# Optimization experiments

Hardware: AMD Instinct MI355X
Metric: run time of the kernel (lower is better)

## Reference

```python
import jax, jax.numpy as jnp
import numpy as np

B, S, E, H, FF = 4, 2048, 1024, 16, 4096
TD = 32  # transition_dim


def _layer_norm(v, g, b, eps=1e-5):
    m = v.mean(-1, keepdims=True)
    var = ((v - m) ** 2).mean(-1, keepdims=True)
    return (v - m) * jax.lax.rsqrt(var + eps) * g + b


def setup_inputs() -> dict:
    key = jax.random.key(0)
    ks = jax.random.split(key, 8)
    w = 0.02
    return {
        "x": jax.random.normal(ks[0], (B, S, E), dtype=jnp.float32),
        "transition_dim": TD,
        "ln1_g": jnp.ones((E,), jnp.float32),
        "ln1_b": jnp.zeros((E,), jnp.float32),
        "ln2_g": jnp.ones((E,), jnp.float32),
        "ln2_b": jnp.zeros((E,), jnp.float32),
        "w_qkv": jax.random.normal(ks[1], (3 * E, E), jnp.float32) * w,
        "b_qkv": jnp.zeros((3 * E,), jnp.float32),
        "w_o": jax.random.normal(ks[2], (E, E), jnp.float32) * w,
        "b_o": jnp.zeros((E,), jnp.float32),
        "w_fc1": jax.random.normal(ks[3], (FF, E), jnp.float32) * w,
        "b_fc1": jnp.zeros((FF,), jnp.float32),
        "w_fc2": jax.random.normal(ks[4], (E, FF), jnp.float32) * w,
        "b_fc2": jnp.zeros((E,), jnp.float32),
    }


def reference(x, transition_dim, ln1_g, ln1_b, ln2_g, ln2_b, w_qkv, b_qkv,
              w_o, b_o, w_fc1, b_fc1, w_fc2, b_fc2):
    Bx, Sx, Ex = x.shape
    Dh = Ex // H
    xn = _layer_norm(x, ln1_g, ln1_b)
    qkv = xn @ w_qkv.T + b_qkv                      # [B,S,3E]
    q, k, v = jnp.split(qkv, 3, axis=-1)
    def heads(t):
        return t.reshape(Bx, Sx, H, Dh).transpose(0, 2, 1, 3)  # [B,H,S,Dh]
    q, k, v = heads(q), heads(k), heads(v)
    scores = jnp.einsum("bhqd,bhkd->bhqk", q, k) / np.sqrt(Dh).astype(np.float32)
    # custom mask: causal (j > i) OR periodic value-column (j % TD == TD-1) blocked
    i = jnp.arange(Sx)
    mask = (i[None, :] > i[:, None]) | ((i[None, :] % transition_dim) == transition_dim - 1)
    scores = jnp.where(mask[None, None], -jnp.inf, scores)
    p = jax.nn.softmax(scores, axis=-1)
    attn = jnp.einsum("bhqk,bhkd->bhqd", p, v)
    attn = attn.transpose(0, 2, 1, 3).reshape(Bx, Sx, Ex)
    attn = attn @ w_o.T + b_o
    x = x + attn
    h = _layer_norm(x, ln2_g, ln2_b)
    h = jax.nn.gelu(h @ w_fc1.T + b_fc1, approximate=False) @ w_fc2.T + b_fc2
    return x + h
```

## Files before the change

kernel.cpp:

```cpp
#include <hip/hip_runtime.h>
#include <hip/hip_bf16.h>

typedef unsigned short u16;
typedef unsigned int u32;
typedef short bf16x8 __attribute__((ext_vector_type(8)));
typedef float f32x4 __attribute__((ext_vector_type(4)));
typedef float f32x16 __attribute__((ext_vector_type(16)));

#define B_ 4
#define S_ 2048
#define E_ 1024
#define H_ 16
#define FF_ 4096
#define M_ 8192

__device__ __forceinline__ u16 f2bf(float f) {
    u32 u = __float_as_uint(f);
    u32 r = (u + 0x7FFFu + ((u >> 16) & 1u)) >> 16;
    return (u16)r;
}
__device__ __forceinline__ float bf2f(u16 v) {
    return __uint_as_float(((u32)v) << 16);
}
__device__ __forceinline__ u32 cvtpk(float lo, float hi) {
    u32 r;
    asm("v_cvt_pk_bf16_f32 %0, %1, %2" : "=v"(r) : "v"(lo), "v"(hi));
    return r;
}
__device__ __forceinline__ void pswap(u32& a, u32& b) {
    asm("v_permlane32_swap_b32 %0, %1" : "+v"(a), "+v"(b));
}

__device__ __forceinline__ void gload16(const void* g, void* l) {
    __builtin_amdgcn_global_load_lds(
        (__attribute__((address_space(1))) void*)g,
        (__attribute__((address_space(3))) void*)l, 16, 0, 0);
}

__global__ __launch_bounds__(256) void cvt_kernel(const float* __restrict__ in,
                                                  u16* __restrict__ out, int n4) {
    int i = blockIdx.x * 256 + threadIdx.x;
    if (i < n4) {
        float4 v = ((const float4*)in)[i];
        ushort4 o;
        o.x = f2bf(v.x); o.y = f2bf(v.y); o.z = f2bf(v.z); o.w = f2bf(v.w);
        ((ushort4*)out)[i] = o;
    }
}

__global__ __launch_bounds__(256) void ln_kernel(const float* __restrict__ x,
                                                 const float* __restrict__ g,
                                                 const float* __restrict__ bb,
                                                 u16* __restrict__ out) {
    int row = blockIdx.x;
    int t = threadIdx.x;
    const float4* xr = (const float4*)(x + (size_t)row * E_);
    float4 v = xr[t];
    float s = v.x + v.y + v.z + v.w;
    float sq = v.x * v.x + v.y * v.y + v.z * v.z + v.w * v.w;
    for (int o = 1; o < 64; o <<= 1) {
        s += __shfl_xor(s, o, 64);
        sq += __shfl_xor(sq, o, 64);
    }
    __shared__ float ss[4], sqs[4];
    int w = t >> 6, l = t & 63;
    if (l == 0) { ss[w] = s; sqs[w] = sq; }
    __syncthreads();
    s = ss[0] + ss[1] + ss[2] + ss[3];
    sq = sqs[0] + sqs[1] + sqs[2] + sqs[3];
    float mean = s * (1.0f / E_);
    float var = sq * (1.0f / E_) - mean * mean;
    float rstd = rsqrtf(var + 1e-5f);
    float4 gv = ((const float4*)g)[t];
    float4 bv = ((const float4*)bb)[t];
    ushort4 o4;
    o4.x = f2bf((v.x - mean) * rstd * gv.x + bv.x);
    o4.y = f2bf((v.y - mean) * rstd * gv.y + bv.y);
    o4.z = f2bf((v.z - mean) * rstd * gv.z + bv.z);
    o4.w = f2bf((v.w - mean) * rstd * gv.w + bv.w);
    ((ushort4*)(out + (size_t)row * E_))[t] = o4;
}

template <int EPI, int BN>
__global__ __launch_bounds__(512, 2) void gemm256(const u16* __restrict__ A,
                                                  const u16* __restrict__ Bt,
                                                  const float* __restrict__ bias,
                                                  void* __restrict__ outp,
                                                  const float* __restrict__ resid,
                                                  int N, int K) {
    constexpr int NF = BN / 64;
    __shared__ u16 ldsA[2 * 2 * 8192];
    __shared__ u16 ldsB[BN == 256 ? 2 * 2 * 8192 : 2 * 8192];
    int t = threadIdx.x;
    int wid = t >> 6, l = t & 63, l15 = l & 15, hi4 = l >> 4;
    int wm = wid >> 2, wn = wid & 3;

    int nwg = gridDim.x;
    int flat = blockIdx.x;
    int swz = (flat & 7) * (nwg >> 3) + (flat >> 3);
    int nx = N / BN;
    int m0 = (swz / nx) * 256, n0 = (swz % nx) * BN;
    const size_t Kb = (size_t)K * 2;

    f32x4 acc[8][NF];
    f32x4 zf = {0.f, 0.f, 0.f, 0.f};
#pragma unroll
    for (int i = 0; i < 8; i++)
#pragma unroll
        for (int j = 0; j < NF; j++) acc[i][j] = zf;

    auto stageA = [&](int buf, int h, int k0) {
#pragma unroll
        for (int rr = 0; rr < 2; ++rr) {
            int o = t * 16 + rr * 8192;
            int lr = o >> 7;
            int gch = ((o >> 4) & 7) ^ (lr & 7);
            int grow = m0 + (lr >> 6) * 128 + h * 64 + (lr & 63);
            gload16((const char*)A + (size_t)grow * Kb + k0 * 2 + gch * 16,
                    (char*)ldsA + (buf * 2 + h) * 16384 + o);
        }
    };
    auto stageB256 = [&](int buf, int h, int k0) {
#pragma unroll
        for (int rr = 0; rr < 2; ++rr) {
            int o = t * 16 + rr * 8192;
            int lr = o >> 7;
            int gch = ((o >> 4) & 7) ^ (lr & 7);
            int grow = n0 + (lr >> 5) * 64 + h * 32 + (lr & 31);
            gload16((const char*)Bt + (size_t)grow * Kb + k0 * 2 + gch * 16,
                    (char*)ldsB + (buf * 2 + h) * 16384 + o);
        }
    };
    auto stageB128 = [&](int buf, int k0) {
#pragma unroll
        for (int rr = 0; rr < 2; ++rr) {
            int o = t * 16 + rr * 8192;
            int lr = o >> 7;
            int gch = ((o >> 4) & 7) ^ (lr & 7);
            int grow = n0 + lr;
            gload16((const char*)Bt + (size_t)grow * Kb + k0 * 2 + gch * 16,
                    (char*)ldsB + buf * 16384 + o);
        }
    };

    auto readA = [&](int bq, int mh, bf16x8 (&af)[4][2]) {
#pragma unroll
        for (int mi = 0; mi < 4; mi++)
#pragma unroll
            for (int ks = 0; ks < 2; ks++) {
                int lr = wm * 64 + mi * 16 + l15;
                int ob = lr * 128 + ks * 64 + hi4 * 16;
                af[mi][ks] = *(const bf16x8*)((const char*)ldsA +
                             (bq * 2 + mh) * 16384 + (ob ^ ((lr & 7) << 4)));
            }
    };
    auto readB256 = [&](int bq, int nh, bf16x8 (&bfr)[2][2]) {
#pragma unroll
        for (int nq = 0; nq < 2; nq++)
#pragma unroll
            for (int ks = 0; ks < 2; ks++) {
                int lr = wn * 32 + nq * 16 + l15;
                int ob = lr * 128 + ks * 64 + hi4 * 16;
                bfr[nq][ks] = *(const bf16x8*)((const char*)ldsB +
                              (bq * 2 + nh) * 16384 + (ob ^ ((lr & 7) << 4)));
            }
    };
    auto readB128 = [&](int bq, bf16x8 (&bfr)[2][2]) {
#pragma unroll
        for (int nq = 0; nq < 2; nq++)
#pragma unroll
            for (int ks = 0; ks < 2; ks++) {
                int lr = wn * 32 + nq * 16 + l15;
                int ob = lr * 128 + ks * 64 + hi4 * 16;
                bfr[nq][ks] = *(const bf16x8*)((const char*)ldsB +
                              bq * 16384 + (ob ^ ((lr & 7) << 4)));
            }
    };
    auto mma = [&](bf16x8 (&af)[4][2], bf16x8 (&bfr)[2][2], int mh, int nh) {
#pragma unroll
        for (int mi = 0; mi < 4; mi++)
#pragma unroll
            for (int nq = 0; nq < 2; nq++)
#pragma unroll
                for (int ks = 0; ks < 2; ks++)
                    acc[mh * 4 + mi][nh * 2 + nq] =
                        __builtin_amdgcn_mfma_f32_16x16x32_bf16(
                            af[mi][ks], bfr[nq][ks], acc[mh * 4 + mi][nh * 2 + nq], 0, 0, 0);
    };

#define GWAIT(N)                                            \
    asm volatile("s_waitcnt vmcnt(" #N ")" ::: "memory");   \
    __builtin_amdgcn_sched_barrier(0);
#define PH_MID                                              \
    __builtin_amdgcn_s_barrier();                           \
    asm volatile("s_waitcnt lgkmcnt(0)" ::: "memory");      \
    __builtin_amdgcn_sched_barrier(0);                      \
    __builtin_amdgcn_s_setprio(1);
#define PH_END                                              \
    __builtin_amdgcn_s_setprio(0);                          \
    __builtin_amdgcn_s_barrier();

    int KT = K >> 6, ITERS = KT >> 1;

    if constexpr (BN == 256) {
        stageB256(0, 0, 0); stageB256(0, 1, 0); stageA(0, 0, 0); stageA(0, 1, 0);
        stageB256(1, 0, 64); stageB256(1, 1, 64); stageA(1, 0, 64);
        GWAIT(6);
        __builtin_amdgcn_s_barrier();
        for (int s = 0; s < ITERS; ++s) {
            int k1 = (2 * s + 1) << 6;
            int k2 = (2 * s + 2) << 6; if (k2 >= K) k2 = 0;
            int k3 = (2 * s + 3) << 6; if (k3 >= K) k3 = 0;
            bf16x8 af[4][2], b0[2][2], b1[2][2];
            readA(0, 0, af); readB256(0, 0, b0); stageA(1, 1, k1);
            PH_MID; mma(af, b0, 0, 0); PH_END;
            readB256(0, 1, b1); stageB256(0, 0, k2);
            PH_MID; mma(af, b1, 0, 1); PH_END;
            readA(0, 1, af); stageB256(0, 1, k2);
            PH_MID; mma(af, b0, 1, 0); PH_END;
            stageA(0, 0, k2); GWAIT(6);
            PH_MID; mma(af, b1, 1, 1); PH_END;
            readA(1, 0, af); readB256(1, 0, b0); stageA(0, 1, k2);
            PH_MID; mma(af, b0, 0, 0); PH_END;
            readB256(1, 1, b1); stageB256(1, 0, k3);
            PH_MID; mma(af, b1, 0, 1); PH_END;
            readA(1, 1, af); stageB256(1, 1, k3);
            PH_MID; mma(af, b0, 1, 0); PH_END;
            stageA(1, 0, k3); GWAIT(6);
            PH_MID; mma(af, b1, 1, 1); PH_END;
        }
    } else {
        stageB128(0, 0); stageA(0, 0, 0); stageA(0, 1, 0);
        stageB128(1, 64); stageA(1, 0, 64);
        GWAIT(4);
        __builtin_amdgcn_s_barrier();
        for (int s = 0; s < ITERS; ++s) {
            int k1 = (2 * s + 1) << 6;
            int k2 = (2 * s + 2) << 6; if (k2 >= K) k2 = 0;
            int k3 = (2 * s + 3) << 6; if (k3 >= K) k3 = 0;
            bf16x8 af[4][2], br[2][2];
            readA(0, 0, af); readB128(0, br); stageA(1, 1, k1);
            PH_MID; mma(af, br, 0, 0); PH_END;
            readA(0, 1, af); stageB128(0, k2); stageA(0, 0, k2); GWAIT(4);
            PH_MID; mma(af, br, 1, 0); PH_END;
            readA(1, 0, af); readB128(1, br); stageA(0, 1, k2);
            PH_MID; mma(af, br, 0, 0); PH_END;
            readA(1, 1, af); stageB128(1, k3); stageA(1, 0, k3); GWAIT(4);
            PH_MID; mma(af, br, 1, 0); PH_END;
        }
    }
#undef GWAIT
#undef PH_MID
#undef PH_END

    float bias_v[NF];
#pragma unroll
    for (int nf = 0; nf < NF; nf++) bias_v[nf] = bias[n0 + wn * (NF * 16) + nf * 16 + l15];

#pragma unroll
    for (int mf = 0; mf < 8; mf++)
#pragma unroll
        for (int nf = 0; nf < NF; nf++)
#pragma unroll
            for (int j = 0; j < 4; j++) {
                int row = m0 + wm * 128 + mf * 16 + hi4 * 4 + j;
                int col = n0 + wn * (NF * 16) + nf * 16 + l15;
                float v = acc[mf][nf][j] + bias_v[nf];
                size_t idx = (size_t)row * N + col;
                if (EPI == 2) v = 0.5f * v * (1.0f + erff(v * 0.70710678118f));
                if (EPI == 1)
                    ((float*)outp)[idx] = resid[idx] + v;
                else
                    ((u16*)outp)[idx] = f2bf(v);
            }
}

__global__ __launch_bounds__(128) void attn_kernel(const u16* __restrict__ qkv,
                                                   u16* __restrict__ aout) {
    __shared__ u16 Ks[64 * 64];
    __shared__ u16 Vt[64 * 64];
    int t = threadIdx.x;
    int wv = t >> 6, l = t & 63;
    int q31 = l & 31, hi = l >> 5;
    int flat = blockIdx.x;
    int logical = (flat & 7) * 256 + (flat >> 3);
    int bh = logical >> 5;
    int qt = 31 - (logical & 31);
    int b = bh >> 4, h = bh & 15;
    int rowq = qt * 64 + wv * 32 + q31;

    const float qs = 0.18033688011f;
    const float THR = 44.3616f;

    bf16x8 qreg[4];
    const u16* qbase = qkv + (size_t)(b * S_ + rowq) * 3072 + h * 64 + hi * 8;
#pragma unroll
    for (int g = 0; g < 4; g++) qreg[g] = *(const bf16x8*)(qbase + 16 * g);

    f32x16 zf16;
#pragma unroll
    for (int r = 0; r < 16; r++) zf16[r] = 0.f;
    f32x16 o0 = zf16, o1 = zf16;
    float mrun = -INFINITY, lrun = 0.f;

    for (int jt = 0; jt <= qt; ++jt) {
        int j0 = jt * 64;
        __syncthreads();
#pragma unroll
        for (int pp = 0; pp < 4; pp++) {
            int oo = 16 * t + 2048 * pp;
            int row = oo >> 7, colb = oo & 127;
            const u16* src = qkv + E_ + (size_t)(b * S_ + j0 + row) * 3072 + h * 64 + (colb >> 1);
            uint4 d16 = *(const uint4*)src;
            int el = (((row << 6) + (colb >> 1)) ^ ((row & 7) << 3));
            *(uint4*)&Ks[el] = d16;
        }
#pragma unroll
        for (int pp = 0; pp < 4; pp++) {
            int db = wv + 2 * pp;
            const u16* src = qkv + 2 * E_ + (size_t)(b * S_ + j0 + l) * 3072 + h * 64 + db * 8;
            uint4 d16 = *(const uint4*)src;
            u32 uu[4] = {d16.x, d16.y, d16.z, d16.w};
#pragma unroll
            for (int e = 0; e < 8; e++) {
                u16 raw = (e & 1) ? (u16)(uu[e >> 1] >> 16) : (u16)(uu[e >> 1] & 0xffffu);
                int d = db * 8 + e;
                Vt[((d << 6) + l) ^ ((d & 7) << 3)] = raw;
            }
        }
        __syncthreads();

        f32x16 s0 = zf16, s1 = zf16;
        __builtin_amdgcn_s_setprio(1);
#pragma unroll
        for (int g = 0; g < 4; g++) {
            int r0 = q31, r1 = 32 + q31;
            bf16x8 k0 = *(const bf16x8*)&Ks[((r0 << 6) + hi * 8 + 16 * g) ^ ((r0 & 7) << 3)];
            bf16x8 k1 = *(const bf16x8*)&Ks[((r1 << 6) + hi * 8 + 16 * g) ^ ((r1 & 7) << 3)];
            s0 = __builtin_amdgcn_mfma_f32_32x32x16_bf16(k0, qreg[g], s0, 0, 0, 0);
            s1 = __builtin_amdgcn_mfma_f32_32x32x16_bf16(k1, qreg[g], s1, 0, 0, 0);
        }
        __builtin_amdgcn_s_setprio(0);

        float mx = -INFINITY;
        int cb0 = j0 + 4 * hi;
        if (jt == qt) {
#pragma unroll
            for (int r = 0; r < 16; r++) {
                const int cc = (r & 3) + 8 * (r >> 2);
                float v0 = s0[r], v1 = s1[r];
                bool bad0 = (cb0 + cc > rowq) || (r == 15 && hi);
                bool bad1 = (cb0 + 32 + cc > rowq) || (r == 15 && hi);
                v0 = bad0 ? -INFINITY : v0;
                v1 = bad1 ? -INFINITY : v1;
                s0[r] = v0; s1[r] = v1;
                mx = fmaxf(mx, fmaxf(v0, v1));
            }
        } else {
#pragma unroll
            for (int r = 0; r < 16; r++) {
                float v0 = s0[r], v1 = s1[r];
                if (r == 15) {
                    v0 = hi ? -INFINITY : v0;
                    v1 = hi ? -INFINITY : v1;
                    s0[r] = v0; s1[r] = v1;
                }
                mx = fmaxf(mx, fmaxf(v0, v1));
            }
        }
        mx = fmaxf(mx, __shfl_xor(mx, 32, 64));

        bool dokeep = __all(mx <= mrun + THR);
        if (!dokeep) {
            float mnew = fmaxf(mrun, mx);
            float sc = __builtin_amdgcn_exp2f((mrun - mnew) * qs);
#pragma unroll
            for (int r = 0; r < 16; r++) { o0[r] *= sc; o1[r] *= sc; }
            lrun *= sc;
            mrun = mnew;
        }
        float mq = mrun * qs;

        float sa = 0.f, sb = 0.f, sc2 = 0.f, sd = 0.f;
#pragma unroll
        for (int r = 0; r < 16; r++) {
            float p0 = __builtin_amdgcn_exp2f(fmaf(s0[r], qs, -mq));
            float p1 = __builtin_amdgcn_exp2f(fmaf(s1[r], qs, -mq));
            s0[r] = p0; s1[r] = p1;
            if (r & 1) { sb += p0; sd += p1; } else { sa += p0; sc2 += p1; }
        }
        lrun += (sa + sb) + (sc2 + sd);

        bf16x8 pa[4];
#pragma unroll
        for (int g = 0; g < 4; g++) {
            const int bs = (g & 1) * 8;
            u32 wa, wb, wc, wd;
            if (g < 2) {
                wa = cvtpk(s0[bs + 0], s0[bs + 1]);
                wb = cvtpk(s0[bs + 4], s0[bs + 5]);
                wc = cvtpk(s0[bs + 2], s0[bs + 3]);
                wd = cvtpk(s0[bs + 6], s0[bs + 7]);
            } else {
                wa = cvtpk(s1[bs + 0], s1[bs + 1]);
                wb = cvtpk(s1[bs + 4], s1[bs + 5]);
                wc = cvtpk(s1[bs + 2], s1[bs + 3]);
                wd = cvtpk(s1[bs + 6], s1[bs + 7]);
            }
            pswap(wa, wb);
            pswap(wc, wd);
            union { u32 w[4]; bf16x8 f; } u;
            u.w[0] = wa; u.w[1] = wc; u.w[2] = wb; u.w[3] = wd;
            pa[g] = u.f;
        }

        __builtin_amdgcn_s_setprio(1);
#pragma unroll
        for (int g = 0; g < 4; g++) {
            int d0 = q31, d1 = 32 + q31;
            bf16x8 v0 = *(const bf16x8*)&Vt[((d0 << 6) + hi * 8 + 16 * g) ^ ((d0 & 7) << 3)];
            bf16x8 v1 = *(const bf16x8*)&Vt[((d1 << 6) + hi * 8 + 16 * g) ^ ((d1 & 7) << 3)];
            o0 = __builtin_amdgcn_mfma_f32_32x32x16_bf16(v0, pa[g], o0, 0, 0, 0);
            o1 = __builtin_amdgcn_mfma_f32_32x32x16_bf16(v1, pa[g], o1, 0, 0, 0);
        }
        __builtin_amdgcn_s_setprio(0);
    }

    lrun += __shfl_xor(lrun, 32, 64);
    float inv = 1.0f / lrun;
    u16* orow = aout + (size_t)(b * S_ + rowq) * E_ + h * 64 + 4 * hi;
#pragma unroll
    for (int r = 0; r < 16; r++) {
        const int cc = (r & 3) + 8 * (r >> 2);
        orow[cc] = f2bf(o0[r] * inv);
        orow[32 + cc] = f2bf(o1[r] * inv);
    }
}

extern "C" void kernel_launch(void* const* d_in, const int* in_sizes, int n_in,
                              void* d_out, int out_size, void* d_ws, size_t ws_size,
                              hipStream_t stream) {
    const float* x = (const float*)d_in[0];
    const float* ln1_g = (const float*)d_in[2];
    const float* ln1_b = (const float*)d_in[3];
    const float* ln2_g = (const float*)d_in[4];
    const float* ln2_b = (const float*)d_in[5];
    const float* w_qkv = (const float*)d_in[6];
    const float* b_qkv = (const float*)d_in[7];
    const float* w_o = (const float*)d_in[8];
    const float* b_o = (const float*)d_in[9];
    const float* w_fc1 = (const float*)d_in[10];
    const float* b_fc1 = (const float*)d_in[11];
    const float* w_fc2 = (const float*)d_in[12];
    const float* b_fc2 = (const float*)d_in[13];
    float* out = (float*)d_out;
    char* ws = (char*)d_ws;

    u16* wqkv_bf = (u16*)(ws);
    u16* wo_bf   = (u16*)(ws + 6291456);
    u16* wfc1_bf = (u16*)(ws + 8388608);
    u16* wfc2_bf = (u16*)(ws + 16777216);
    u16* xn_bf   = (u16*)(ws + 25165824);
    u16* qkv_bf  = (u16*)(ws + 41943040);
    u16* ffn1_bf = (u16*)(ws + 41943040);
    u16* attn_bf = (u16*)(ws + 92274688);
    float* x2    = (float*)(ws + 109051904);
    (void)in_sizes; (void)n_in; (void)out_size; (void)ws_size;

    cvt_kernel<<<3072, 256, 0, stream>>>(w_qkv, wqkv_bf, 786432);
    cvt_kernel<<<1024, 256, 0, stream>>>(w_o, wo_bf, 262144);
    cvt_kernel<<<4096, 256, 0, stream>>>(w_fc1, wfc1_bf, 1048576);
    cvt_kernel<<<4096, 256, 0, stream>>>(w_fc2, wfc2_bf, 1048576);

    ln_kernel<<<M_, 256, 0, stream>>>(x, ln1_g, ln1_b, xn_bf);

    gemm256<0, 256><<<384, 512, 0, stream>>>(xn_bf, wqkv_bf, b_qkv, qkv_bf, nullptr, 3072, 1024);

    attn_kernel<<<2048, 128, 0, stream>>>(qkv_bf, attn_bf);

    gemm256<1, 128><<<256, 512, 0, stream>>>(attn_bf, wo_bf, b_o, x2, x, 1024, 1024);

    ln_kernel<<<M_, 256, 0, stream>>>(x2, ln2_g, ln2_b, xn_bf);

    gemm256<2, 256><<<512, 512, 0, stream>>>(xn_bf, wfc1_bf, b_fc1, ffn1_bf, nullptr, 4096, 1024);

    gemm256<1, 128><<<256, 512, 0, stream>>>(ffn1_bf, wfc2_bf, b_fc2, out, x2, 1024, 4096);
}
```

Measured before the change: 404.6 us.

## Emit transposed V from QKV GEMM and double-buffer async K/V loads in attention

The QKV GEMM gets a new epilogue that also writes V in a transposed [B,H,Dh,S] layout into workspace (aliased with x2, which is only written after attention). The attention kernel drops its per-element V transpose into LDS and synchronous K loads. It now uses global_load_lds into double-buffered K/V tiles, prefetching two tiles ahead with vmcnt waits and barriers. This aims to overlap memory latency with MFMA work and remove scalar LDS scatter stores. The cost is extra global writes in the GEMM epilogue and twice the LDS per block.

```diff
diff --git a/kernel.cpp b/kernel.cpp
--- a/kernel.cpp
+++ b/kernel.cpp
@@ -30,7 +30,6 @@
 __device__ __forceinline__ void pswap(u32& a, u32& b) {
     asm("v_permlane32_swap_b32 %0, %1" : "+v"(a), "+v"(b));
 }
-
 __device__ __forceinline__ void gload16(const void* g, void* l) {
     __builtin_amdgcn_global_load_lds(
         (__attribute__((address_space(1))) void*)g,
@@ -87,6 +86,7 @@
                                                   const float* __restrict__ bias,
                                                   void* __restrict__ outp,
                                                   const float* __restrict__ resid,
+                                                  u16* __restrict__ vt,
                                                   int N, int K) {
     constexpr int NF = BN / 64;
     __shared__ u16 ldsA[2 * 2 * 8192];
@@ -257,28 +257,52 @@
 #pragma unroll
     for (int nf = 0; nf < NF; nf++) bias_v[nf] = bias[n0 + wn * (NF * 16) + nf * 16 + l15];
 
-#pragma unroll
-    for (int mf = 0; mf < 8; mf++)
-#pragma unroll
-        for (int nf = 0; nf < NF; nf++)
-#pragma unroll
-            for (int j = 0; j < 4; j++) {
-                int row = m0 + wm * 128 + mf * 16 + hi4 * 4 + j;
+    if constexpr (EPI == 3) {
+#pragma unroll
+        for (int mf = 0; mf < 8; mf++)
+#pragma unroll
+            for (int nf = 0; nf < NF; nf++) {
                 int col = n0 + wn * (NF * 16) + nf * 16 + l15;
-                float v = acc[mf][nf][j] + bias_v[nf];
-                size_t idx = (size_t)row * N + col;
-                if (EPI == 2) v = 0.5f * v * (1.0f + erff(v * 0.70710678118f));
-                if (EPI == 1)
-                    ((float*)outp)[idx] = resid[idx] + v;
-                else
-                    ((u16*)outp)[idx] = f2bf(v);
-            }
+                int row0 = m0 + wm * 128 + mf * 16 + hi4 * 4;
+                ushort4 sv;
+                u16* o16 = (u16*)outp;
+#pragma unroll
+                for (int j = 0; j < 4; j++) {
+                    float v = acc[mf][nf][j] + bias_v[nf];
+                    u16 r = f2bf(v);
+                    o16[(size_t)(row0 + j) * N + col] = r;
+                    ((u16*)&sv)[j] = r;
+                }
+                if (col >= 2048) {
+                    int bb = row0 >> 11, s0r = row0 & 2047;
+                    *(ushort4*)&vt[(((size_t)(bb << 10) + (col - 2048)) << 11) + s0r] = sv;
+                }
+            }
+    } else {
+#pragma unroll
+        for (int mf = 0; mf < 8; mf++)
+#pragma unroll
+            for (int nf = 0; nf < NF; nf++)
+#pragma unroll
+                for (int j = 0; j < 4; j++) {
+                    int row = m0 + wm * 128 + mf * 16 + hi4 * 4 + j;
+                    int col = n0 + wn * (NF * 16) + nf * 16 + l15;
+                    float v = acc[mf][nf][j] + bias_v[nf];
+                    size_t idx = (size_t)row * N + col;
+                    if (EPI == 2) v = 0.5f * v * (1.0f + erff(v * 0.70710678118f));
+                    if (EPI == 1)
+                        ((float*)outp)[idx] = resid[idx] + v;
+                    else
+                        ((u16*)outp)[idx] = f2bf(v);
+                }
+    }
 }
 
 __global__ __launch_bounds__(128) void attn_kernel(const u16* __restrict__ qkv,
+                                                   const u16* __restrict__ vt,
                                                    u16* __restrict__ aout) {
-    __shared__ u16 Ks[64 * 64];
-    __shared__ u16 Vt[64 * 64];
+    __shared__ u16 Ksb[2 * 4096];
+    __shared__ u16 Vsb[2 * 4096];
     int t = threadIdx.x;
     int wv = t >> 6, l = t & 63;
     int q31 = l & 31, hi = l >> 5;
@@ -297,46 +321,50 @@
 #pragma unroll
     for (int g = 0; g < 4; g++) qreg[g] = *(const bf16x8*)(qbase + 16 * g);
 
+    const char* srcK0 = (const char*)(qkv + E_ + (size_t)(b * S_ + (t >> 3)) * 3072 + h * 64) +
+                        ((t & 7) ^ ((t >> 3) & 7)) * 16;
+    const char* srcV0 = (const char*)(vt + ((size_t)(bh * 64 + (t >> 3))) * 2048) +
+                        ((t & 7) ^ ((t >> 3) & 7)) * 16;
+    auto issueK = [&](int buf, int j0) {
+#pragma unroll
+        for (int pp = 0; pp < 4; pp++)
+            gload16(srcK0 + (size_t)pp * 98304 + (size_t)j0 * 6144,
+                    (char*)Ksb + buf * 8192 + 16 * t + 2048 * pp);
+    };
+    auto issueV = [&](int buf, int j0) {
+#pragma unroll
+        for (int pp = 0; pp < 4; pp++)
+            gload16(srcV0 + (size_t)pp * 65536 + (size_t)j0 * 2,
+                    (char*)Vsb + buf * 8192 + 16 * t + 2048 * pp);
+    };
+
     f32x16 zf16;
 #pragma unroll
     for (int r = 0; r < 16; r++) zf16[r] = 0.f;
     f32x16 o0 = zf16, o1 = zf16;
     float mrun = -INFINITY, lrun = 0.f;
 
+    int j1 = (qt >= 1) ? 64 : 0;
+    issueK(0, 0); issueV(0, 0);
+    issueK(1, j1); issueV(1, j1);
+
     for (int jt = 0; jt <= qt; ++jt) {
+        int cur = jt & 1;
         int j0 = jt * 64;
-        __syncthreads();
-#pragma unroll
-        for (int pp = 0; pp < 4; pp++) {
-            int oo = 16 * t + 2048 * pp;
-            int row = oo >> 7, colb = oo & 127;
-            const u16* src = qkv + E_ + (size_t)(b * S_ + j0 + row) * 3072 + h * 64 + (colb >> 1);
-            uint4 d16 = *(const uint4*)src;
-            int el = (((row << 6) + (colb >> 1)) ^ ((row & 7) << 3));
-            *(uint4*)&Ks[el] = d16;
-        }
-#pragma unroll
-        for (int pp = 0; pp < 4; pp++) {
-            int db = wv + 2 * pp;
-            const u16* src = qkv + 2 * E_ + (size_t)(b * S_ + j0 + l) * 3072 + h * 64 + db * 8;
-            uint4 d16 = *(const uint4*)src;
-            u32 uu[4] = {d16.x, d16.y, d16.z, d16.w};
-#pragma unroll
-            for (int e = 0; e < 8; e++) {
-                u16 raw = (e & 1) ? (u16)(uu[e >> 1] >> 16) : (u16)(uu[e >> 1] & 0xffffu);
-                int d = db * 8 + e;
-                Vt[((d << 6) + l) ^ ((d & 7) << 3)] = raw;
-            }
-        }
-        __syncthreads();
+        asm volatile("s_waitcnt vmcnt(8)" ::: "memory");
+        __builtin_amdgcn_sched_barrier(0);
+        __builtin_amdgcn_s_barrier();
+
+        const u16* Kc = Ksb + cur * 4096;
+        const u16* Vc = Vsb + cur * 4096;
 
         f32x16 s0 = zf16, s1 = zf16;
         __builtin_amdgcn_s_setprio(1);
 #pragma unroll
         for (int g = 0; g < 4; g++) {
             int r0 = q31, r1 = 32 + q31;
-            bf16x8 k0 = *(const bf16x8*)&Ks[((r0 << 6) + hi * 8 + 16 * g) ^ ((r0 & 7) << 3)];
-            bf16x8 k1 = *(const bf16x8*)&Ks[((r1 << 6) + hi * 8 + 16 * g) ^ ((r1 & 7) << 3)];
+            bf16x8 k0 = *(const bf16x8*)&Kc[((r0 << 6) + hi * 8 + 16 * g) ^ ((r0 & 7) << 3)];
+            bf16x8 k1 = *(const bf16x8*)&Kc[((r1 << 6) + hi * 8 + 16 * g) ^ ((r1 & 7) << 3)];
             s0 = __builtin_amdgcn_mfma_f32_32x32x16_bf16(k0, qreg[g], s0, 0, 0, 0);
             s1 = __builtin_amdgcn_mfma_f32_32x32x16_bf16(k1, qreg[g], s1, 0, 0, 0);
         }
@@ -418,12 +446,17 @@
 #pragma unroll
         for (int g = 0; g < 4; g++) {
             int d0 = q31, d1 = 32 + q31;
-            bf16x8 v0 = *(const bf16x8*)&Vt[((d0 << 6) + hi * 8 + 16 * g) ^ ((d0 & 7) << 3)];
-            bf16x8 v1 = *(const bf16x8*)&Vt[((d1 << 6) + hi * 8 + 16 * g) ^ ((d1 & 7) << 3)];
+            bf16x8 v0 = *(const bf16x8*)&Vc[((d0 << 6) + hi * 8 + 16 * g) ^ ((d0 & 7) << 3)];
+            bf16x8 v1 = *(const bf16x8*)&Vc[((d1 << 6) + hi * 8 + 16 * g) ^ ((d1 & 7) << 3)];
             o0 = __builtin_amdgcn_mfma_f32_32x32x16_bf16(v0, pa[g], o0, 0, 0, 0);
             o1 = __builtin_amdgcn_mfma_f32_32x32x16_bf16(v1, pa[g], o1, 0, 0, 0);
         }
         __builtin_amdgcn_s_setprio(0);
+
+        __builtin_amdgcn_s_barrier();
+        int nj = (jt + 2 <= qt) ? (jt + 2) * 64 : 0;
+        issueK(cur, nj);
+        issueV(cur, nj);
     }
 
     lrun += __shfl_xor(lrun, 32, 64);
@@ -465,6 +498,7 @@
     u16* ffn1_bf = (u16*)(ws + 41943040);
     u16* attn_bf = (u16*)(ws + 92274688);
     float* x2    = (float*)(ws + 109051904);
+    u16* vtw     = (u16*)(ws + 109051904);
     (void)in_sizes; (void)n_in; (void)out_size; (void)ws_size;
 
     cvt_kernel<<<3072, 256, 0, stream>>>(w_qkv, wqkv_bf, 786432);
@@ -474,15 +508,15 @@
 
     ln_kernel<<<M_, 256, 0, stream>>>(x, ln1_g, ln1_b, xn_bf);
 
-    gemm256<0, 256><<<384, 512, 0, stream>>>(xn_bf, wqkv_bf, b_qkv, qkv_bf, nullptr, 3072, 1024);
-
-    attn_kernel<<<2048, 128, 0, stream>>>(qkv_bf, attn_bf);
-
-    gemm256<1, 128><<<256, 512, 0, stream>>>(attn_bf, wo_bf, b_o, x2, x, 1024, 1024);
+    gemm256<3, 256><<<384, 512, 0, stream>>>(xn_bf, wqkv_bf, b_qkv, qkv_bf, nullptr, vtw, 3072, 1024);
+
+    attn_kernel<<<2048, 128, 0, stream>>>(qkv_bf, vtw, attn_bf);
+
+    gemm256<1, 128><<<256, 512, 0, stream>>>(attn_bf, wo_bf, b_o, x2, x, nullptr, 1024, 1024);
 
     ln_kernel<<<M_, 256, 0, stream>>>(x2, ln2_g, ln2_b, xn_bf);
 
-    gemm256<2, 256><<<512, 512, 0, stream>>>(xn_bf, wfc1_bf, b_fc1, ffn1_bf, nullptr, 4096, 1024);
-
-    gemm256<1, 128><<<256, 512, 0, stream>>>(ffn1_bf, wfc2_bf, b_fc2, out, x2, 1024, 4096);
-}
+    gemm256<2, 256><<<512, 512, 0, stream>>>(xn_bf, wfc1_bf, b_fc1, ffn1_bf, nullptr, nullptr, 4096, 1024);
+
+    gemm256<1, 128><<<256, 512, 0, stream>>>(ffn1_bf, wfc2_bf, b_fc2, out, x2, nullptr, 1024, 4096);
+}
```

New measurement: 407.5 us. No clear change (+0.7%).
